# Kernel optimization log

Hardware: AMD Instinct MI355X
Metric: run time of the kernel (lower is better)

## Reference

```python
import jax, jax.numpy as jnp
import numpy as np

EPS_DIAG = 1e-4
EPS_SOFT = 1e-5
SCALE_DIV = 100000.0


def _cov2cor(x):
    # x: [N, C, d, d]; scale rows and cols by 1/sqrt(|diag|) (== D^-1 @ x @ D^-1)
    dia = jnp.abs(jnp.diagonal(x, axis1=-2, axis2=-1))          # [N, C, d]
    inv = 1.0 / jnp.sqrt(jnp.maximum(dia, EPS_DIAG))
    cor = x * inv[..., :, None] * inv[..., None, :]
    return jnp.clip(cor, -1.0, 1.0)


def _soft_pd_max(x):
    # x: [N, C, d, d]
    x = x - jnp.max(x, axis=(2, 3), keepdims=True)
    e = jnp.exp(x)
    dia = jnp.sum(e, axis=-1)                                    # [N, C, d]
    dia = jnp.maximum(dia, jnp.sum(dia, axis=2, keepdims=True) / SCALE_DIV)
    dia = jnp.maximum(dia, EPS_SOFT)
    inv = 1.0 / jnp.sqrt(dia)
    return e * inv[..., :, None] * inv[..., None, :]


def setup_inputs() -> dict:
    key = jax.random.key(0)
    k0, k1, k2, k3 = jax.random.split(key, 4)
    N, C, d = 64, 64, 64
    inputs = jax.random.normal(k0, (N, C, d, d), dtype=jnp.float32)
    # NonNeg uniform [0, 2/C] init for queries/keys
    w_queries = jax.random.uniform(k1, (C, C), dtype=jnp.float32, minval=0.0, maxval=2.0 / C)
    w_keys = jax.random.uniform(k2, (C, C), dtype=jnp.float32, minval=0.0, maxval=2.0 / C)
    # values: |N(0, 1/sqrt(C))| column-L1-normalized
    wv = jnp.abs(jax.random.normal(k3, (C, C), dtype=jnp.float32) / jnp.sqrt(jnp.float32(C)))
    w_values = wv / jnp.sum(wv, axis=0)
    return {"inputs": inputs, "w_queries": w_queries, "w_keys": w_keys, "w_values": w_values}


def reference(inputs, w_queries, w_keys, w_values):
    cor = _cov2cor(inputs)                                       # [N, C, d, d]
    X = jnp.transpose(cor, (0, 2, 3, 1))                         # [N, d, d, C]
    XWQ = jnp.matmul(X, w_queries)                               # [N, d, d, C]
    XWK = jnp.matmul(X, w_keys)
    XWV = jnp.matmul(X, w_values)
    XWQt = jnp.transpose(XWQ, (0, 3, 1, 2))                      # [N, C, d, d]
    XWKt = jnp.transpose(XWK, (0, 3, 2, 1))                      # [N, C, d, d] (transposed within dxd)
    XWKT = jnp.transpose(XWK, (0, 3, 1, 2))
    A_pre = jnp.matmul(jnp.matmul(XWKt, XWQt), XWKT)             # [N, C, d, d]
    A = _soft_pd_max(A_pre)
    V = jnp.transpose(XWV, (0, 3, 1, 2))                         # [N, C, d, d]
    AXA = jnp.matmul(jnp.matmul(A, V), jnp.transpose(A, (0, 1, 3, 2)))
    return inputs + AXA
```

## Files before the change

kernel.cpp:

```cpp
#include <hip/hip_runtime.h>

#define PITCH 72
#define QKV_STRIDE 12288

typedef __attribute__((ext_vector_type(8))) short short8v;
typedef __attribute__((ext_vector_type(4))) short short4v;
typedef __attribute__((ext_vector_type(4))) float f32x4;

__device__ __forceinline__ short f2bf(float v) {
    unsigned u = __builtin_bit_cast(unsigned, v);
    unsigned r = (u + 0x7FFFu + ((u >> 16) & 1u)) >> 16;
    return (short)r;
}
__device__ __forceinline__ float bf2f(short s) {
    unsigned u = ((unsigned)(unsigned short)s) << 16;
    return __builtin_bit_cast(float, u);
}

#define MFMA(a, b, c) __builtin_amdgcn_mfma_f32_16x16x32_bf16(a, b, c, 0, 0, 0)

__device__ __forceinline__ short8v ldfrag(const short* p, int rowtile, int kc, int l) {
    return *(const short8v*)&p[(rowtile * 16 + (l & 15)) * PITCH + kc * 32 + (l >> 4) * 8];
}
__device__ __forceinline__ short8v gfrag(const short* __restrict__ p, int rowtile, int kc, int l) {
    return *(const short8v*)&p[(rowtile * 16 + (l & 15)) * 64 + kc * 32 + (l >> 4) * 8];
}
__device__ __forceinline__ short8v gfrag_s(const short* __restrict__ p, int rowtile,
                                           int kc, int l, int stride) {
    return *(const short8v*)&p[(rowtile * 16 + (l & 15)) * stride + kc * 32 + (l >> 4) * 8];
}

__device__ __forceinline__ void p1(const short* xh, const short* yh,
                                   int w, int l, f32x4 (&acc)[4]) {
#pragma unroll
    for (int ct = 0; ct < 4; ++ct) acc[ct] = (f32x4){0.f, 0.f, 0.f, 0.f};
#pragma unroll
    for (int kc = 0; kc < 2; ++kc) {
        short8v aH = ldfrag(xh, w, kc, l);
#pragma unroll
        for (int ct = 0; ct < 4; ++ct)
            acc[ct] = MFMA(aH, ldfrag(yh, ct, kc, l), acc[ct]);
    }
}

__device__ __forceinline__ void p1_g(const short* __restrict__ xg, const short* yh,
                                     int w, int l, f32x4 (&acc)[4]) {
#pragma unroll
    for (int ct = 0; ct < 4; ++ct) acc[ct] = (f32x4){0.f, 0.f, 0.f, 0.f};
#pragma unroll
    for (int kc = 0; kc < 2; ++kc) {
        short8v aH = gfrag_s(xg, w, kc, l, QKV_STRIDE);
#pragma unroll
        for (int ct = 0; ct < 4; ++ct)
            acc[ct] = MFMA(aH, ldfrag(yh, ct, kc, l), acc[ct]);
    }
}

__device__ __forceinline__ void pack1(const f32x4 (&acc)[4], short* zh, int w, int l) {
    int m0 = w * 16 + (l >> 4) * 4;
#pragma unroll
    for (int ct = 0; ct < 4; ++ct) {
        int n = ct * 16 + (l & 15);
        short4v h;
#pragma unroll
        for (int r = 0; r < 4; ++r) h[r] = f2bf(acc[ct][r]);
        *(short4v*)&zh[n * PITCH + m0] = h;
    }
}

__device__ __forceinline__ void idtrans_ip1(short* pa, int w, int l) {
    short8v a0 = ldfrag(pa, w, 0, l);
    short8v a1 = ldfrag(pa, w, 1, l);
    short8v I0, I1;
#pragma unroll
    for (int j = 0; j < 8; ++j) {
        int bit = 8 * (l >> 4) + j;
        I0[j] = (bit == (l & 15))      ? (short)0x3F80 : (short)0;
        I1[j] = (bit == (l & 15) + 16) ? (short)0x3F80 : (short)0;
    }
    __syncthreads();
    int m0 = w * 16 + (l >> 4) * 4;
    const f32x4 z4 = {0.f, 0.f, 0.f, 0.f};
#pragma unroll
    for (int s = 0; s < 4; ++s) {
        f32x4 d = MFMA((s >> 1) ? a1 : a0, (s & 1) ? I1 : I0, z4);
        short4v ha;
#pragma unroll
        for (int r = 0; r < 4; ++r) ha[r] = f2bf(d[r]);
        *(short4v*)&pa[(s * 16 + (l & 15)) * PITCH + m0] = ha;
    }
}

__global__ __launch_bounds__(256) void k0_prep(const float* __restrict__ x,
                                               const float* __restrict__ wq,
                                               const float* __restrict__ wk,
                                               const float* __restrict__ wv,
                                               float* __restrict__ invd,
                                               short* __restrict__ w3h) {
    int b = blockIdx.x;
    if (b < 1024) {
        int t = b * 256 + threadIdx.x;
        int nc = t >> 6, k = t & 63;
        float v = fabsf(x[(size_t)nc * 4096 + (size_t)k * 65]);
        invd[t] = rsqrtf(fmaxf(v, 1e-4f));
    } else {
        int idx = (b - 1024) * 256 + threadIdx.x;
        int co = idx >> 6, c = idx & 63;
        const float* w = (co < 64) ? wq : (co < 128) ? wk : wv;
        w3h[idx] = f2bf(w[c * 64 + (co & 63)]);
    }
}

__global__ __launch_bounds__(256, 6) void k1_mix_mfma(
    const float* __restrict__ x, const float* __restrict__ invd,
    const short* __restrict__ w3h,
    short* __restrict__ QKV)
{
    __shared__ __align__(16) short smem[6912];
    short* ch = smem;

    const int b = blockIdx.x, n = b >> 6, i = b & 63;
    const int t = threadIdx.x, l = t & 63, w = t >> 6;
    const size_t nbase = (size_t)n * 64;

#pragma unroll
    for (int rep = 0; rep < 4; ++rep) {
        int id = rep * 256 + t;
        int c = id >> 4, j4 = (id & 15) * 4;
        float4 xv = *(const float4*)&x[((nbase + c) * 64 + i) * 64 + j4];
        float ii = invd[(nbase + c) * 64 + i];
        float4 jv = *(const float4*)&invd[(nbase + c) * 64 + j4];
        float vv[4] = {xv.x * ii * jv.x, xv.y * ii * jv.y,
                       xv.z * ii * jv.z, xv.w * ii * jv.w};
        short4v h;
#pragma unroll
        for (int r = 0; r < 4; ++r)
            h[r] = f2bf(fminf(1.0f, fmaxf(-1.0f, vv[r])));
        *(short4v*)&ch[c * PITCH + j4] = h;
    }
    __syncthreads();
    idtrans_ip1(ch, w, l);
    __syncthreads();

    f32x4 acc[4][3];
#pragma unroll
    for (int jt = 0; jt < 4; ++jt)
#pragma unroll
        for (int cc = 0; cc < 3; ++cc) acc[jt][cc] = (f32x4){0.f, 0.f, 0.f, 0.f};
#pragma unroll
    for (int kc = 0; kc < 2; ++kc) {
        short8v aH[4];
#pragma unroll
        for (int jt = 0; jt < 4; ++jt) aH[jt] = ldfrag(ch, jt, kc, l);
#pragma unroll
        for (int cc = 0; cc < 3; ++cc) {
            short8v bH = gfrag(w3h, w * 3 + cc, kc, l);
#pragma unroll
            for (int jt = 0; jt < 4; ++jt)
                acc[jt][cc] = MFMA(aH[jt], bH, acc[jt][cc]);
        }
    }
    __syncthreads();

    const int m0 = (l >> 4) * 4, nb = l & 15;
    short* dst = QKV + (size_t)b * QKV_STRIDE;

    if (w < 2) {
#pragma unroll
        for (int cc = 0; cc < 3; ++cc) {
            int zrow = (w * 3 + cc) * 16 + nb;
#pragma unroll
            for (int jt = 0; jt < 4; ++jt) {
                short4v h;
#pragma unroll
                for (int r = 0; r < 4; ++r) h[r] = f2bf(acc[jt][cc][r]);
                *(short4v*)&smem[zrow * PITCH + jt * 16 + m0] = h;
            }
        }
    }
    __syncthreads();
#pragma unroll
    for (int rep = 0; rep < 3; ++rep) {
        int id = rep * 256 + t;
        *(short8v*)&dst[id * 8] = *(short8v*)&smem[(id >> 3) * PITCH + (id & 7) * 8];
    }
    __syncthreads();

    if (w >= 2) {
#pragma unroll
        for (int cc = 0; cc < 3; ++cc) {
            int zrow = ((w - 2) * 3 + cc) * 16 + nb;
#pragma unroll
            for (int jt = 0; jt < 4; ++jt) {
                short4v h;
#pragma unroll
                for (int r = 0; r < 4; ++r) h[r] = f2bf(acc[jt][cc][r]);
                *(short4v*)&smem[zrow * PITCH + jt * 16 + m0] = h;
            }
        }
    }
    __syncthreads();
#pragma unroll
    for (int rep = 0; rep < 3; ++rep) {
        int id = rep * 256 + t;
        *(short8v*)&dst[6144 + id * 8] =
            *(short8v*)&smem[(id >> 3) * PITCH + (id & 7) * 8];
    }
}

__global__ __launch_bounds__(256, 5) void k2_attn_mfma(
    const float* __restrict__ x,
    const short* __restrict__ QKV,
    float* __restrict__ out)
{
    __shared__ __align__(16) short P[2][4608];
    __shared__ float part[4][64];
    __shared__ float invs[64];
    __shared__ float red[4];

    const int t = threadIdx.x, l = t & 63, w = t >> 6;
    const int nc = blockIdx.x, n = nc >> 6, c = nc & 63;
    const size_t gbase = (size_t)nc * 4096;

    const short* qh = QKV + (size_t)n * 64 * QKV_STRIDE + (size_t)c * 64;
    const short* kh = qh + 64 * 64;
    const short* vh = qh + 128 * 64;

#pragma unroll
    for (int rep = 0; rep < 4; ++rep) {
        int id = rep * 256 + t;
        int r = id >> 4, c4 = (id & 15) * 4;
        *(short4v*)&P[0][r * PITCH + c4] =
            *(const short4v*)&kh[r * QKV_STRIDE + c4];
    }
    __syncthreads();

    idtrans_ip1(P[0], w, l);
    __syncthreads();

    f32x4 acc[4];

    p1_g(qh, P[0], w, l, acc);
    pack1(acc, P[1], w, l);
    __syncthreads();

    p1(P[1], P[0], w, l, acc);

    float mx = -1e30f;
#pragma unroll
    for (int ct = 0; ct < 4; ++ct)
#pragma unroll
        for (int r = 0; r < 4; ++r) mx = fmaxf(mx, acc[ct][r]);
#pragma unroll
    for (int off = 1; off < 64; off <<= 1) mx = fmaxf(mx, __shfl_xor(mx, off));
    if (l == 0) red[w] = mx;
    __syncthreads();
    mx = fmaxf(fmaxf(red[0], red[1]), fmaxf(red[2], red[3]));

    float e[4][4];
    float cs[4];
#pragma unroll
    for (int ct = 0; ct < 4; ++ct) {
        float s = 0.f;
#pragma unroll
        for (int r = 0; r < 4; ++r) {
            float ev = __expf(acc[ct][r] - mx);
            e[ct][r] = ev;
            s += ev;
        }
        cs[ct] = s;
    }
#pragma unroll
    for (int ct = 0; ct < 4; ++ct) {
        cs[ct] += __shfl_xor(cs[ct], 16);
        cs[ct] += __shfl_xor(cs[ct], 32);
    }
    if (l < 16) {
#pragma unroll
        for (int ct = 0; ct < 4; ++ct) part[w][ct * 16 + l] = cs[ct];
    }
    __syncthreads();
    if (t < 64) {
        float dia = part[0][t] + part[1][t] + part[2][t] + part[3][t];
        float tot = dia;
#pragma unroll
        for (int off = 1; off < 64; off <<= 1) tot += __shfl_xor(tot, off);
        dia = fmaxf(dia, tot / 100000.0f);
        dia = fmaxf(dia, 1e-5f);
        invs[t] = rsqrtf(dia);
    }
    __syncthreads();

    {
        int m0 = w * 16 + (l >> 4) * 4;
        float ir[4] = {invs[m0], invs[m0 + 1], invs[m0 + 2], invs[m0 + 3]};
        int nb = l & 15;
#pragma unroll
        for (int ct = 0; ct < 4; ++ct) {
            float ic = invs[ct * 16 + nb];
            short4v h;
#pragma unroll
            for (int r = 0; r < 4; ++r)
                h[r] = f2bf(e[ct][r] * ir[r] * ic);
            *(short4v*)&P[1][(ct * 16 + nb) * PITCH + m0] = h;
        }
    }
    __syncthreads();

    p1_g(vh, P[1], w, l, acc);
    pack1(acc, P[0], w, l);
    __syncthreads();

    p1(P[1], P[0], w, l, acc);
    __syncthreads();

    {
        float* ofs = (float*)&P[0][0];
        int m0 = w * 16 + (l >> 4) * 4;
        int nb = l & 15;
#pragma unroll
        for (int ct = 0; ct < 4; ++ct)
#pragma unroll
            for (int r = 0; r < 4; ++r)
                ofs[(m0 + r) * 68 + ct * 16 + nb] = acc[ct][r];
    }
    __syncthreads();
    {
        const float* ofs = (const float*)&P[0][0];
#pragma unroll
        for (int rep = 0; rep < 4; ++rep) {
            int id = rep * 256 + t;
            int row = id >> 4, c4 = (id & 15) * 4;
            float4 v  = *(const float4*)&ofs[row * 68 + c4];
            float4 xv = *(const float4*)&x[gbase + (size_t)row * 64 + c4];
            *(float4*)&out[gbase + (size_t)row * 64 + c4] =
                make_float4(xv.x + v.x, xv.y + v.y, xv.z + v.z, xv.w + v.w);
        }
    }
}

extern "C" void kernel_launch(void* const* d_in, const int* in_sizes, int n_in,
                              void* d_out, int out_size, void* d_ws, size_t ws_size,
                              hipStream_t stream) {
    const float* x  = (const float*)d_in[0];
    const float* wq = (const float*)d_in[1];
    const float* wk = (const float*)d_in[2];
    const float* wv = (const float*)d_in[3];
    float* out = (float*)d_out;

    char* wsb = (char*)d_ws;
    float* invd = (float*)wsb;
    short* w3h  = (short*)(wsb + (1 << 20));
    short* QKV  = (short*)(wsb + (2 << 20));

    k0_prep<<<1072, 256, 0, stream>>>(x, wq, wk, wv, invd, w3h);
    k1_mix_mfma<<<4096, 256, 0, stream>>>(x, invd, w3h, QKV);
    k2_attn_mfma<<<4096, 256, 0, stream>>>(x, QKV, out);
}
```

Before: 90.23 us.

## Rewrite mix kernel as single-wave blocks without barriers, transposing via identity MFMA

The QKV mixing kernel now runs as 64-thread single-wave blocks instead of 256-thread blocks, so every __syncthreads is dropped. The in-place transpose is done with MFMAs against identity fragments, and the output is produced in six sequential chunks through a separate LDS staging area. This removes barrier stalls and cross-wave coordination. In exchange, each wave does four times more global loads, MFMAs and stores serially, and occupancy now depends on the LDS footprint per single-wave block.

```diff
diff --git a/kernel.cpp b/kernel.cpp
--- a/kernel.cpp
+++ b/kernel.cpp
@@ -111,21 +111,22 @@
     }
 }
 
-__global__ __launch_bounds__(256, 6) void k1_mix_mfma(
+__global__ __launch_bounds__(64) void k1_mix_wave(
     const float* __restrict__ x, const float* __restrict__ invd,
     const short* __restrict__ w3h,
     short* __restrict__ QKV)
 {
     __shared__ __align__(16) short smem[6912];
     short* ch = smem;
+    short* z  = smem + 4608;
 
     const int b = blockIdx.x, n = b >> 6, i = b & 63;
-    const int t = threadIdx.x, l = t & 63, w = t >> 6;
+    const int l = threadIdx.x;
     const size_t nbase = (size_t)n * 64;
 
 #pragma unroll
-    for (int rep = 0; rep < 4; ++rep) {
-        int id = rep * 256 + t;
+    for (int rep = 0; rep < 16; ++rep) {
+        int id = rep * 64 + l;
         int c = id >> 4, j4 = (id & 15) * 4;
         float4 xv = *(const float4*)&x[((nbase + c) * 64 + i) * 64 + j4];
         float ii = invd[(nbase + c) * 64 + i];
@@ -138,73 +139,74 @@
             h[r] = f2bf(fminf(1.0f, fmaxf(-1.0f, vv[r])));
         *(short4v*)&ch[c * PITCH + j4] = h;
     }
-    __syncthreads();
-    idtrans_ip1(ch, w, l);
-    __syncthreads();
-
-    f32x4 acc[4][3];
-#pragma unroll
-    for (int jt = 0; jt < 4; ++jt)
-#pragma unroll
-        for (int cc = 0; cc < 3; ++cc) acc[jt][cc] = (f32x4){0.f, 0.f, 0.f, 0.f};
-#pragma unroll
-    for (int kc = 0; kc < 2; ++kc) {
-        short8v aH[4];
-#pragma unroll
-        for (int jt = 0; jt < 4; ++jt) aH[jt] = ldfrag(ch, jt, kc, l);
-#pragma unroll
-        for (int cc = 0; cc < 3; ++cc) {
-            short8v bH = gfrag(w3h, w * 3 + cc, kc, l);
-#pragma unroll
-            for (int jt = 0; jt < 4; ++jt)
-                acc[jt][cc] = MFMA(aH[jt], bH, acc[jt][cc]);
-        }
-    }
-    __syncthreads();
-
-    const int m0 = (l >> 4) * 4, nb = l & 15;
+
+    short8v f[4][2];
+#pragma unroll
+    for (int tile = 0; tile < 4; ++tile)
+#pragma unroll
+        for (int kc = 0; kc < 2; ++kc)
+            f[tile][kc] = ldfrag(ch, tile, kc, l);
+    short8v I0, I1;
+#pragma unroll
+    for (int j = 0; j < 8; ++j) {
+        int bit = 8 * (l >> 4) + j;
+        I0[j] = (bit == (l & 15))      ? (short)0x3F80 : (short)0;
+        I1[j] = (bit == (l & 15) + 16) ? (short)0x3F80 : (short)0;
+    }
+    const f32x4 zz = {0.f, 0.f, 0.f, 0.f};
+#pragma unroll
+    for (int tile = 0; tile < 4; ++tile) {
+        int m0 = tile * 16 + (l >> 4) * 4;
+#pragma unroll
+        for (int s = 0; s < 4; ++s) {
+            f32x4 d = MFMA(f[tile][s >> 1], (s & 1) ? I1 : I0, zz);
+            short4v ha;
+#pragma unroll
+            for (int r = 0; r < 4; ++r) ha[r] = f2bf(d[r]);
+            *(short4v*)&ch[(s * 16 + (l & 15)) * PITCH + m0] = ha;
+        }
+    }
+
+    const int m0p = (l >> 4) * 4, nb = l & 15;
     short* dst = QKV + (size_t)b * QKV_STRIDE;
-
-    if (w < 2) {
-#pragma unroll
-        for (int cc = 0; cc < 3; ++cc) {
-            int zrow = (w * 3 + cc) * 16 + nb;
+#pragma unroll
+    for (int q = 0; q < 6; ++q) {
+        f32x4 acc[4][2];
+#pragma unroll
+        for (int jt = 0; jt < 4; ++jt)
+#pragma unroll
+            for (int cc = 0; cc < 2; ++cc)
+                acc[jt][cc] = (f32x4){0.f, 0.f, 0.f, 0.f};
+#pragma unroll
+        for (int kc = 0; kc < 2; ++kc) {
+            short8v aH[4];
+#pragma unroll
+            for (int jt = 0; jt < 4; ++jt) aH[jt] = ldfrag(ch, jt, kc, l);
+#pragma unroll
+            for (int cc = 0; cc < 2; ++cc) {
+                short8v bH = gfrag(w3h, q * 2 + cc, kc, l);
+#pragma unroll
+                for (int jt = 0; jt < 4; ++jt)
+                    acc[jt][cc] = MFMA(aH[jt], bH, acc[jt][cc]);
+            }
+        }
+#pragma unroll
+        for (int cc = 0; cc < 2; ++cc) {
+            int zrow = cc * 16 + nb;
 #pragma unroll
             for (int jt = 0; jt < 4; ++jt) {
                 short4v h;
 #pragma unroll
                 for (int r = 0; r < 4; ++r) h[r] = f2bf(acc[jt][cc][r]);
-                *(short4v*)&smem[zrow * PITCH + jt * 16 + m0] = h;
+                *(short4v*)&z[zrow * PITCH + jt * 16 + m0p] = h;
             }
         }
-    }
-    __syncthreads();
-#pragma unroll
-    for (int rep = 0; rep < 3; ++rep) {
-        int id = rep * 256 + t;
-        *(short8v*)&dst[id * 8] = *(short8v*)&smem[(id >> 3) * PITCH + (id & 7) * 8];
-    }
-    __syncthreads();
-
-    if (w >= 2) {
-#pragma unroll
-        for (int cc = 0; cc < 3; ++cc) {
-            int zrow = ((w - 2) * 3 + cc) * 16 + nb;
-#pragma unroll
-            for (int jt = 0; jt < 4; ++jt) {
-                short4v h;
-#pragma unroll
-                for (int r = 0; r < 4; ++r) h[r] = f2bf(acc[jt][cc][r]);
-                *(short4v*)&smem[zrow * PITCH + jt * 16 + m0] = h;
-            }
-        }
-    }
-    __syncthreads();
-#pragma unroll
-    for (int rep = 0; rep < 3; ++rep) {
-        int id = rep * 256 + t;
-        *(short8v*)&dst[6144 + id * 8] =
-            *(short8v*)&smem[(id >> 3) * PITCH + (id & 7) * 8];
+#pragma unroll
+        for (int rep = 0; rep < 4; ++rep) {
+            int id = rep * 64 + l;
+            *(short8v*)&dst[q * 2048 + id * 8] =
+                *(short8v*)&z[(id >> 3) * PITCH + (id & 7) * 8];
+        }
     }
 }
 
@@ -354,6 +356,6 @@
     short* QKV  = (short*)(wsb + (2 << 20));
 
     k0_prep<<<1072, 256, 0, stream>>>(x, wq, wk, wv, invd, w3h);
-    k1_mix_mfma<<<4096, 256, 0, stream>>>(x, invd, w3h, QKV);
+    k1_mix_wave<<<4096, 64, 0, stream>>>(x, invd, w3h, QKV);
     k2_attn_mfma<<<4096, 256, 0, stream>>>(x, QKV, out);
 }
```

After: 82.69 us. -8.4%, faster.
